# Kernel tuning notes

Measured on AMD Instinct MI355X. Metric: run time of the kernel, lower is better.

## Reference

```python
import jax, jax.numpy as jnp
import numpy as np
from jax import lax

D_MODEL = 512; N_HEADS = 32; HEAD_DIM = 16
D_INNER = 1024; D_STATE = 64; HDIM = 64; NH = 16; D_CONV = 4
CONV_CH = D_INNER + 2 * D_STATE          # 1152
D_INPROJ = 2 * D_INNER + 2 * D_STATE + NH  # 2192
B, L = 4, 1024


def setup_inputs() -> dict:
    key = jax.random.key(0)
    ks = jax.random.split(key, 16)
    def rn(k, shape, scale=0.02):
        return jax.random.normal(k, shape, jnp.float32) * scale
    inp = {"h": jax.random.normal(ks[0], (B, L, D_MODEL), jnp.float32)}
    inp["attn_in_w"] = rn(ks[1], (3 * D_MODEL, D_MODEL))
    inp["attn_in_b"] = jnp.zeros((3 * D_MODEL,), jnp.float32)
    inp["attn_out_w"] = rn(ks[2], (D_MODEL, D_MODEL))
    inp["attn_out_b"] = jnp.zeros((D_MODEL,), jnp.float32)
    i = 3
    for p in ("fwd", "bwd"):
        inp[f"{p}_inproj_w"] = rn(ks[i], (D_INPROJ, D_MODEL)); i += 1
        inp[f"{p}_conv_w"] = rn(ks[i], (CONV_CH, D_CONV), 0.1); i += 1
        inp[f"{p}_conv_b"] = jnp.zeros((CONV_CH,), jnp.float32)
        inp[f"{p}_dt_bias"] = rn(ks[i], (NH,), 0.5); i += 1
        inp[f"{p}_A_log"] = jnp.log(jax.random.uniform(ks[i], (NH,), jnp.float32, 1.0, 16.0)); i += 1
        inp[f"{p}_D"] = jnp.ones((NH,), jnp.float32)
        inp[f"{p}_norm_w"] = jnp.ones((D_INNER,), jnp.float32)
        inp[f"{p}_outproj_w"] = rn(ks[i], (D_MODEL, D_INNER)); i += 1
    inp["ln_w"] = jnp.ones((D_MODEL,), jnp.float32)
    inp["ln_b"] = jnp.zeros((D_MODEL,), jnp.float32)
    return inp


def _mha(h, in_w, in_b, out_w, out_b):
    b, l, d = h.shape
    qkv = h @ in_w.T + in_b
    q, k, v = jnp.split(qkv, 3, axis=-1)
    def heads(t):
        return t.reshape(b, l, N_HEADS, HEAD_DIM).transpose(0, 2, 1, 3)
    q, k, v = heads(q), heads(k), heads(v)
    scores = jnp.einsum('bhqd,bhkd->bhqk', q, k) * (1.0 / np.sqrt(HEAD_DIM))
    attn = jax.nn.softmax(scores, axis=-1)
    o = jnp.einsum('bhqk,bhkd->bhqd', attn, v).transpose(0, 2, 1, 3).reshape(b, l, d)
    return o @ out_w.T + out_b


def _causal_dwconv(x, w, bias):
    # x: (b, l, c), w: (c, k) depthwise causal conv
    xt = x.transpose(0, 2, 1)  # (b, c, l)
    out = lax.conv_general_dilated(xt, w[:, None, :], (1,), [(D_CONV - 1, 0)],
                                   feature_group_count=CONV_CH,
                                   dimension_numbers=('NCH', 'OIH', 'NCH'))
    return (out + bias[None, :, None]).transpose(0, 2, 1)


def _ssd(x, dt, A, Bm, Cm):
    # x: (b,l,nh,p), dt: (b,l,nh), Bm/Cm: (b,l,n) (ngroups=1)
    b = x.shape[0]
    dA = jnp.exp(dt * A)          # (b,l,nh)
    dtx = dt[..., None] * x       # (b,l,nh,p)
    def step(hst, inp):
        dA_t, dtx_t, B_t, C_t = inp
        hst = dA_t[:, :, None, None] * hst + dtx_t[..., None] * B_t[:, None, None, :]
        return hst, jnp.einsum('bhpn,bn->bhp', hst, C_t)
    init = jnp.zeros((b, NH, HDIM, D_STATE), x.dtype)
    _, ys = lax.scan(step, init, (dA.transpose(1, 0, 2), dtx.transpose(1, 0, 2, 3),
                                  Bm.transpose(1, 0, 2), Cm.transpose(1, 0, 2)))
    return ys.transpose(1, 0, 2, 3)  # (b,l,nh,p)


def _mamba2(u, inproj_w, conv_w, conv_b, dt_bias, A_log, Dp, norm_w, outproj_w):
    b, l, _ = u.shape
    zxbcdt = u @ inproj_w.T                      # (b,l,2192)
    z = zxbcdt[..., :D_INNER]
    xBC = zxbcdt[..., D_INNER:D_INNER + CONV_CH]
    dt = jax.nn.softplus(zxbcdt[..., D_INNER + CONV_CH:] + dt_bias)  # (b,l,nh)
    xBC = jax.nn.silu(_causal_dwconv(xBC, conv_w, conv_b))
    x = xBC[..., :D_INNER].reshape(b, l, NH, HDIM)
    Bm = xBC[..., D_INNER:D_INNER + D_STATE]
    Cm = xBC[..., D_INNER + D_STATE:]
    A = -jnp.exp(A_log)
    y = _ssd(x, dt, A, Bm, Cm) + Dp[None, None, :, None] * x
    y = y.reshape(b, l, D_INNER) * jax.nn.silu(z)  # gated (norm_before_gate=False)
    y = y * lax.rsqrt(jnp.mean(y * y, axis=-1, keepdims=True) + 1e-5) * norm_w  # RMSNormGated
    return y @ outproj_w.T


def reference(h, attn_in_w, attn_in_b, attn_out_w, attn_out_b,
              fwd_inproj_w, fwd_conv_w, fwd_conv_b, fwd_dt_bias, fwd_A_log, fwd_D, fwd_norm_w, fwd_outproj_w,
              bwd_inproj_w, bwd_conv_w, bwd_conv_b, bwd_dt_bias, bwd_A_log, bwd_D, bwd_norm_w, bwd_outproj_w,
              ln_w, ln_b):
    attn_out = _mha(h, attn_in_w, attn_in_b, attn_out_w, attn_out_b)
    fwd_out = _mamba2(h, fwd_inproj_w, fwd_conv_w, fwd_conv_b, fwd_dt_bias, fwd_A_log, fwd_D, fwd_norm_w, fwd_outproj_w)
    bwd_out = jnp.flip(_mamba2(jnp.flip(h, 1), bwd_inproj_w, bwd_conv_w, bwd_conv_b, bwd_dt_bias, bwd_A_log, bwd_D, bwd_norm_w, bwd_outproj_w), 1)
    s = h + attn_out + fwd_out + bwd_out
    mu = jnp.mean(s, axis=-1, keepdims=True)
    var = jnp.mean((s - mu) ** 2, axis=-1, keepdims=True)
    return (s - mu) * lax.rsqrt(var + 1e-5) * ln_w + ln_b
```

## Files before the change

kernel.cpp:

```cpp
#include <hip/hip_runtime.h>
#include <math.h>
#include <stdint.h>

#define B_ 4
#define L_ 1024
#define DM 512
#define NHA 32
#define HD 16
#define DI 1024
#define DSTATE 64
#define HDIM_ 64
#define NHM 16
#define DCONV 4
#define CONVCH 1152
#define DINPROJ 2192
#define NTOK (B_*L_)
#define QC 64
#define NC (L_/QC)
#define QKVS 5920

typedef __bf16 bf16x8 __attribute__((ext_vector_type(8)));
typedef float f32x4 __attribute__((ext_vector_type(4)));
typedef unsigned short ushort8 __attribute__((ext_vector_type(8)));
typedef unsigned short ushort4v __attribute__((ext_vector_type(4)));
typedef __fp16 fp16x2 __attribute__((ext_vector_type(2)));
typedef _Float16 f16x4 __attribute__((ext_vector_type(4)));
typedef _Float16 f16x8 __attribute__((ext_vector_type(8)));

__device__ __forceinline__ float siluf(float x) {
    return x / (1.0f + __expf(-x));
}

__device__ __forceinline__ unsigned short f2bf(float f) {
    unsigned u = __float_as_uint(f);
    unsigned r = (u + 0x7FFFu + ((u >> 16) & 1u)) >> 16;
    return (unsigned short)r;
}

__device__ __forceinline__ float bf2f(unsigned short u) {
    return __uint_as_float((unsigned)u << 16);
}

__device__ __forceinline__ void cvt8(const float* src, unsigned short* dst) {
    float4 a = ((const float4*)src)[0];
    float4 b = ((const float4*)src)[1];
    ushort8 o;
    o[0] = f2bf(a.x); o[1] = f2bf(a.y); o[2] = f2bf(a.z); o[3] = f2bf(a.w);
    o[4] = f2bf(b.x); o[5] = f2bf(b.y); o[6] = f2bf(b.z); o[7] = f2bf(b.w);
    *(ushort8*)dst = o;
}

__device__ __forceinline__ void gload16(const void* g, void* l) {
    auto gp = reinterpret_cast<const __attribute__((address_space(1))) unsigned int*>(
        reinterpret_cast<uintptr_t>(g));
    auto lp = reinterpret_cast<__attribute__((address_space(3))) unsigned int*>(
        reinterpret_cast<uintptr_t>(l));
    __builtin_amdgcn_global_load_lds(gp, lp, 16, 0, 0);
}

#define S0 262144
#define S1 (S0 + 98304)
#define S2 (S1 + 32768)
#define S3 (S2 + 140288)
#define S4 (S3 + 140288)
__global__ void cvt_all_kernel(const float* __restrict__ h, unsigned short* __restrict__ hB,
                               const float* __restrict__ w1, unsigned short* __restrict__ d1,
                               const float* __restrict__ w2, unsigned short* __restrict__ d2,
                               const float* __restrict__ w3, unsigned short* __restrict__ d3,
                               const float* __restrict__ w4, unsigned short* __restrict__ d4) {
    int i = blockIdx.x * blockDim.x + threadIdx.x;
    const float* src; unsigned short* dst; int off;
    if (i < S0)      { src = h;  dst = hB; off = i; }
    else if (i < S1) { src = w1; dst = d1; off = i - S0; }
    else if (i < S2) { src = w2; dst = d2; off = i - S1; }
    else if (i < S3) { src = w3; dst = d3; off = i - S2; }
    else             { src = w4; dst = d4; off = i - S3; }
    cvt8(src + (size_t)off * 8, dst + (size_t)off * 8);
}

__global__ void cvt_outproj_kernel(const float* __restrict__ fw, const float* __restrict__ bw,
                                   unsigned short* __restrict__ dst) {
    int i = blockIdx.x * blockDim.x + threadIdx.x;
    const int n8 = DM * DI / 8;
    int half = i >= n8;
    int off = half ? i - n8 : i;
    const float* src = half ? bw : fw;
    int e = off * 8;
    int r = e / DI, c = e % DI;
    cvt8(src + e, dst + (size_t)r * 2048 + half * 1024 + c);
}

template <int BN, bool OBF16, bool SWZ>
__global__ __launch_bounds__(256) void gemm_mfma_staged(
        const unsigned short* __restrict__ Ab, const unsigned short* __restrict__ Wb,
        const float* __restrict__ bias, int biasN, void* __restrict__ Cout,
        int M, int N, int K) {
    constexpr int BM = 128, BK = 32;
    constexpr int NF = BN / 32;
    constexpr int BLOADS = BN / 64;
    __shared__ unsigned short As[2][BM * BK];
    __shared__ unsigned short Bs[2][BN * BK];

    const int tid = threadIdx.x;
    const int wave = tid >> 6, lane = tid & 63;
    const int l15 = lane & 15, g = lane >> 4;
    const int wm = wave >> 1, wn = wave & 1;
    int m0, n0;
    if constexpr (SWZ) {
        int d = blockIdx.x;
        int xcd = d & 7, jj = d >> 3;
        n0 = (xcd * 6 + jj % 6) * BN;
        m0 = (jj / 6) * BM;
    } else {
        m0 = blockIdx.y * BM;
        n0 = blockIdx.x * BN;
    }

    f32x4 acc[4][NF];
    #pragma unroll
    for (int mi = 0; mi < 4; ++mi)
        #pragma unroll
        for (int nj = 0; nj < NF; ++nj) acc[mi][nj] = (f32x4){0.f, 0.f, 0.f, 0.f};

    auto stage = [&](int bufi, int k0) {
        #pragma unroll
        for (int i = 0; i < 2; ++i) {
            int c = (wave * 2 + i) * 64 + lane;
            int row = c >> 2;
            int kc = ((c & 3) ^ (row & 3)) * 8;
            gload16(Ab + (size_t)(m0 + row) * K + k0 + kc,
                    &As[bufi][(wave * 2 + i) * 64 * 8]);
        }
        #pragma unroll
        for (int i = 0; i < BLOADS; ++i) {
            int c = (wave * BLOADS + i) * 64 + lane;
            int row = c >> 2;
            int kc = ((c & 3) ^ (row & 3)) * 8;
            int rn = n0 + row; if (rn >= N) rn = N - 1;
            gload16(Wb + (size_t)rn * K + k0 + kc,
                    &Bs[bufi][(wave * BLOADS + i) * 64 * 8]);
        }
    };

    int cur = 0;
    stage(0, 0);
    __syncthreads();
    for (int k0 = 0; k0 < K; k0 += BK) {
        if (k0 + BK < K) stage(cur ^ 1, k0 + BK);
        const unsigned short* Ac = As[cur];
        const unsigned short* Bc = Bs[cur];
        bf16x8 af[4];
        #pragma unroll
        for (int mi = 0; mi < 4; ++mi) {
            int ar = wm * 64 + mi * 16 + l15;
            af[mi] = *(const bf16x8*)(Ac + ar * BK + ((g ^ (ar & 3)) * 8));
        }
        bf16x8 bfr[NF];
        #pragma unroll
        for (int nj = 0; nj < NF; ++nj) {
            int br = wn * (BN / 2) + nj * 16 + l15;
            bfr[nj] = *(const bf16x8*)(Bc + br * BK + ((g ^ (br & 3)) * 8));
        }
        #pragma unroll
        for (int mi = 0; mi < 4; ++mi)
            #pragma unroll
            for (int nj = 0; nj < NF; ++nj)
                acc[mi][nj] = __builtin_amdgcn_mfma_f32_16x16x32_bf16(af[mi], bfr[nj], acc[mi][nj], 0, 0, 0);
        __syncthreads();
        cur ^= 1;
    }

    #pragma unroll
    for (int mi = 0; mi < 4; ++mi) {
        int rbase = m0 + wm * 64 + mi * 16 + g * 4;
        #pragma unroll
        for (int nj = 0; nj < NF; ++nj) {
            int col = n0 + wn * (BN / 2) + nj * 16 + l15;
            if (col < N) {
                float bv = (bias && col < biasN) ? bias[col] : 0.f;
                #pragma unroll
                for (int r = 0; r < 4; ++r) {
                    float v = acc[mi][nj][r] + bv;
                    if constexpr (OBF16)
                        ((unsigned short*)Cout)[(size_t)(rbase + r) * N + col] = f2bf(v);
                    else
                        ((float*)Cout)[(size_t)(rbase + r) * N + col] = v;
                }
            }
        }
    }
}

#define KP 24
#define VP 132
__global__ __launch_bounds__(256) void attn_mfma_kernel(const unsigned short* __restrict__ qkv,
                                                        unsigned short* __restrict__ ob) {
    const int n = blockIdx.x;
    const int xcd = n & 7;
    const int j = n >> 3;
    const int bh = ((j >> 4) << 3) + xcd;
    const int qt = j & 15;
    const int h = bh & 31;
    const int b = bh >> 5;
    const int tid = threadIdx.x;
    const int wave = tid >> 6, lane = tid & 63;
    const int l15 = lane & 15, g = lane >> 4;

    __shared__ _Float16 Ksm[128 * KP];
    __shared__ _Float16 VsmT[16 * VP];

    const unsigned short* base = qkv + (size_t)b * L_ * QKVS;
    const int qrow = qt * 64 + wave * 16 + l15;

    f16x4 qf;
    {
        ushort4v qv = *(const ushort4v*)(base + (size_t)qrow * QKVS + h * 16 + g * 4);
        fp16x2 qa = __builtin_amdgcn_cvt_pkrtz(bf2f(qv[0]) * 0.25f, bf2f(qv[1]) * 0.25f);
        fp16x2 qb = __builtin_amdgcn_cvt_pkrtz(bf2f(qv[2]) * 0.25f, bf2f(qv[3]) * 0.25f);
        qf[0] = (_Float16)qa[0]; qf[1] = (_Float16)qa[1];
        qf[2] = (_Float16)qb[0]; qf[3] = (_Float16)qb[1];
    }
    f32x4 yacc = (f32x4){0.f, 0.f, 0.f, 0.f};
    float s = 0.f;

    const int sk = tid >> 1;
    const int sd = (tid & 1) * 8;

    for (int c0 = 0; c0 < L_; c0 += 128) {
        {
            ushort8 ka = *(const ushort8*)(base + (size_t)(c0 + sk) * QKVS + 512 + h * 16 + sd);
            fp16x2 k0 = __builtin_amdgcn_cvt_pkrtz(bf2f(ka[0]), bf2f(ka[1]));
            fp16x2 k1 = __builtin_amdgcn_cvt_pkrtz(bf2f(ka[2]), bf2f(ka[3]));
            fp16x2 k2 = __builtin_amdgcn_cvt_pkrtz(bf2f(ka[4]), bf2f(ka[5]));
            fp16x2 k3 = __builtin_amdgcn_cvt_pkrtz(bf2f(ka[6]), bf2f(ka[7]));
            f16x8 kv;
            kv[0] = (_Float16)k0[0]; kv[1] = (_Float16)k0[1];
            kv[2] = (_Float16)k1[0]; kv[3] = (_Float16)k1[1];
            kv[4] = (_Float16)k2[0]; kv[5] = (_Float16)k2[1];
            kv[6] = (_Float16)k3[0]; kv[7] = (_Float16)k3[1];
            *(f16x8*)(&Ksm[sk * KP + sd]) = kv;
            ushort8 va = *(const ushort8*)(base + (size_t)(c0 + sk) * QKVS + 1024 + h * 16 + sd);
            #pragma unroll
            for (int jj = 0; jj < 8; ++jj)
                VsmT[(sd + jj) * VP + sk] = (_Float16)bf2f(va[jj]);
        }
        __syncthreads();
        #pragma unroll
        for (int half = 0; half < 2; ++half) {
            f32x4 st[4];
            #pragma unroll
            for (int ks = 0; ks < 4; ++ks) {
                f16x4 kf = *(const f16x4*)(&Ksm[((half * 4 + ks) * 16 + l15) * KP + g * 4]);
                st[ks] = __builtin_amdgcn_mfma_f32_16x16x16f16(kf, qf, (f32x4){0.f,0.f,0.f,0.f}, 0, 0, 0);
            }
            float p[16];
            float cs = 0.f;
            #pragma unroll
            for (int ks = 0; ks < 4; ++ks) {
                #pragma unroll
                for (int r = 0; r < 4; ++r) {
                    p[ks * 4 + r] = __expf(st[ks][r]);
                    cs += p[ks * 4 + r];
                }
            }
            cs += __shfl_xor(cs, 16);
            cs += __shfl_xor(cs, 32);
            s += cs;
            #pragma unroll
            for (int ks = 0; ks < 4; ++ks) {
                fp16x2 plo = __builtin_amdgcn_cvt_pkrtz(p[ks*4+0], p[ks*4+1]);
                fp16x2 phi = __builtin_amdgcn_cvt_pkrtz(p[ks*4+2], p[ks*4+3]);
                f16x4 pf;
                pf[0] = (_Float16)plo[0]; pf[1] = (_Float16)plo[1];
                pf[2] = (_Float16)phi[0]; pf[3] = (_Float16)phi[1];
                f16x4 vf = *(const f16x4*)(&VsmT[l15 * VP + (half * 4 + ks) * 16 + g * 4]);
                yacc = __builtin_amdgcn_mfma_f32_16x16x16f16(vf, pf, yacc, 0, 0, 0);
            }
        }
        __syncthreads();
    }
    float inv = 1.f / s;
    ushort4v o;
    o[0] = f2bf(yacc[0] * inv);
    o[1] = f2bf(yacc[1] * inv);
    o[2] = f2bf(yacc[2] * inv);
    o[3] = f2bf(yacc[3] * inv);
    *(ushort4v*)(ob + (size_t)(b * L_ + qrow) * 512 + h * 16 + g * 4) = o;
}

__global__ void conv_silu_kernel(const unsigned short* __restrict__ megaA,
                                 const float* __restrict__ cw0, const float* __restrict__ cb0,
                                 const float* __restrict__ cw1, const float* __restrict__ cb1,
                                 unsigned short* __restrict__ out) {
    const int rev = blockIdx.y;
    const float* conv_w = rev ? cw1 : cw0;
    const float* conv_b = rev ? cb1 : cb0;
    int idx = blockIdx.x * blockDim.x + threadIdx.x;
    if (idx >= NTOK * (CONVCH / 4)) return;
    int c4 = (idx % (CONVCH / 4)) * 4;
    int bl = idx / (CONVCH / 4);
    int l = bl % L_;
    int b = bl / L_;
    const unsigned short* src = megaA + (size_t)b * L_ * QKVS + 1536 + rev * DINPROJ + 1024 + c4;
    float4 w0 = *(const float4*)(conv_w + (c4 + 0) * 4);
    float4 w1 = *(const float4*)(conv_w + (c4 + 1) * 4);
    float4 w2 = *(const float4*)(conv_w + (c4 + 2) * 4);
    float4 w3 = *(const float4*)(conv_w + (c4 + 3) * 4);
    float4 acc = *(const float4*)(conv_b + c4);
    const float wt[4][4] = {{w0.x, w0.y, w0.z, w0.w}, {w1.x, w1.y, w1.z, w1.w},
                            {w2.x, w2.y, w2.z, w2.w}, {w3.x, w3.y, w3.z, w3.w}};
    #pragma unroll
    for (int j = 0; j < 4; ++j) {
        int ll = rev ? (l + 3 - j) : (l - 3 + j);
        if (ll >= 0 && ll < L_) {
            ushort4v x = *(const ushort4v*)(src + (size_t)ll * QKVS);
            acc.x = fmaf(wt[0][j], bf2f(x[0]), acc.x);
            acc.y = fmaf(wt[1][j], bf2f(x[1]), acc.y);
            acc.z = fmaf(wt[2][j], bf2f(x[2]), acc.z);
            acc.w = fmaf(wt[3][j], bf2f(x[3]), acc.w);
        }
    }
    ushort4v o;
    o[0] = f2bf(siluf(acc.x)); o[1] = f2bf(siluf(acc.y));
    o[2] = f2bf(siluf(acc.z)); o[3] = f2bf(siluf(acc.w));
    *(ushort4v*)(out + (size_t)rev * NTOK * CONVCH + (size_t)bl * CONVCH + c4) = o;
}

__global__ void dt_exact_kernel(const float* __restrict__ h,
                                const float* __restrict__ wdt0, const float* __restrict__ bias0,
                                const float* __restrict__ wdt1, const float* __restrict__ bias1,
                                float* __restrict__ dt) {
    const int dir = blockIdx.y;
    const float* wdt = dir ? wdt1 : wdt0;
    const float* dbias = dir ? bias1 : bias0;
    const int row = blockIdx.x;
    const int tid = threadIdx.x;
    const int g = tid >> 4, j = tid & 15;
    const float* hr = h + (size_t)row * DM;
    const float* wr = wdt + (size_t)g * DM;
    float s = 0.f;
    #pragma unroll 8
    for (int t = 0; t < 32; ++t) {
        int k = j + t * 16;
        s = fmaf(hr[k], wr[k], s);
    }
    s += __shfl_xor(s, 1); s += __shfl_xor(s, 2);
    s += __shfl_xor(s, 4); s += __shfl_xor(s, 8);
    if (j == 0) {
        float v = s + dbias[g];
        dt[(size_t)dir * NTOK * NHM + (size_t)row * NHM + g] = (v > 20.f) ? v : log1pf(__expf(v));
    }
}

__global__ __launch_bounds__(256) void ssd_chunk_kernel(
        const unsigned short* __restrict__ xbcAll, const float* __restrict__ dtAll,
        const float* __restrict__ Al0, const float* __restrict__ Dp0,
        const float* __restrict__ Al1, const float* __restrict__ Dp1,
        unsigned short* __restrict__ y16, float* __restrict__ Sb0, float* __restrict__ Sb1,
        float* __restrict__ Edec) {
    const int dir = blockIdx.y;
    const int rev = dir;
    const unsigned short* xbc = xbcAll + (size_t)dir * NTOK * CONVCH;
    const float* dtb = dtAll + (size_t)dir * NTOK * NHM;
    float* Sbuf = dir ? Sb1 : Sb0;
    unsigned short* y = y16 + (size_t)dir * NTOK * DI;

    const int bid = blockIdx.x;
    const int q = bid & (NC - 1);
    const int bh = bid / NC;
    const int b = bh >> 4, h = bh & 15;
    const int tid = threadIdx.x;
    const int wave = tid >> 6, lane = tid & 63;
    const int l15 = lane & 15, l4 = lane >> 4;

    __shared__ unsigned short Bn[64 * 72];
    __shared__ unsigned short Cn[64 * 72];
    __shared__ unsigned short Btw[64 * 72];
    __shared__ unsigned short Gt[64 * 72];
    __shared__ unsigned short xT[64 * 72];
    __shared__ float sdt[QC], sc[QC], wsv[QC];

    const float A = -__expf((dir ? Al1 : Al0)[h]);
    const float Dh = (dir ? Dp1 : Dp0)[h];
    const int r = tid >> 2, qq = tid & 3;

    #pragma unroll
    for (int j = 0; j < 4; ++j) {
        int qd = qq + j * 4;
        int t = q * QC + r;
        int l = rev ? (L_ - 1 - t) : t;
        const unsigned short* rowp = xbc + (size_t)(b * L_ + l) * CONVCH;
        *(ushort4v*)&Bn[r * 72 + qd * 4] = *(const ushort4v*)(rowp + 1024 + qd * 4);
        *(ushort4v*)&Cn[r * 72 + qd * 4] = *(const ushort4v*)(rowp + 1088 + qd * 4);
    }
    if (tid < QC) {
        int t = q * QC + tid;
        int l = rev ? (L_ - 1 - t) : t;
        sdt[tid] = dtb[(size_t)(b * L_ + l) * NHM + h];
    }
    __syncthreads();
    if (tid == 0) {
        float run = 0.f;
        for (int i = 0; i < QC; ++i) { run += A * sdt[i]; sc[i] = run; }
    }
    __syncthreads();
    if (tid < QC) wsv[tid] = sdt[tid] * __expf(sc[QC - 1] - sc[tid]);
    if (tid == 0) Edec[dir * 1024 + bid] = __expf(sc[QC - 1]);
    __syncthreads();

    {
        int n = tid >> 2, s0 = (tid & 3) * 16;
        ushort8 o0, o1;
        #pragma unroll
        for (int k = 0; k < 8; ++k) {
            o0[k] = f2bf(bf2f(Bn[(s0 + k) * 72 + n]) * wsv[s0 + k]);
            o1[k] = f2bf(bf2f(Bn[(s0 + 8 + k) * 72 + n]) * wsv[s0 + 8 + k]);
        }
        *(ushort8*)&Btw[n * 72 + s0] = o0;
        *(ushort8*)&Btw[n * 72 + s0 + 8] = o1;
    }
    #pragma unroll
    for (int j = 0; j < 4; ++j) {
        int qd = qq + j * 4;
        int t = q * QC + r;
        int l = rev ? (L_ - 1 - t) : t;
        const unsigned short* rowp = xbc + (size_t)(b * L_ + l) * CONVCH + h * 64;
        ushort4v xv = *(const ushort4v*)(rowp + qd * 4);
        xT[(qd * 4 + 0) * 72 + r] = xv[0];
        xT[(qd * 4 + 1) * 72 + r] = xv[1];
        xT[(qd * 4 + 2) * 72 + r] = xv[2];
        xT[(qd * 4 + 3) * 72 + r] = xv[3];
    }
    __syncthreads();

    f32x4 accG[4];
    #pragma unroll
    for (int j = 0; j < 4; ++j) accG[j] = (f32x4){0.f, 0.f, 0.f, 0.f};
    #pragma unroll
    for (int k0 = 0; k0 < 64; k0 += 32) {
        bf16x8 af = *(const bf16x8*)&Bn[(wave * 16 + l15) * 72 + l4 * 8 + k0];
        #pragma unroll
        for (int j = 0; j < 4; ++j) {
            bf16x8 bfj = *(const bf16x8*)&Cn[(j * 16 + l15) * 72 + l4 * 8 + k0];
            accG[j] = __builtin_amdgcn_mfma_f32_16x16x32_bf16(af, bfj, accG[j], 0, 0, 0);
        }
    }
    #pragma unroll
    for (int j = 0; j < 4; ++j) {
        #pragma unroll
        for (int rr = 0; rr < 4; ++rr) {
            int s = wave * 16 + l4 * 4 + rr;
            int i = j * 16 + l15;
            float g = (s <= i) ? accG[j][rr] * sdt[s] * __expf(sc[i] - sc[s]) : 0.f;
            Gt[i * 72 + s] = f2bf(g);
        }
    }
    __syncthreads();

    {
        f32x4 accY[4];
        #pragma unroll
        for (int j = 0; j < 4; ++j) accY[j] = (f32x4){0.f, 0.f, 0.f, 0.f};
        #pragma unroll
        for (int k0 = 0; k0 < 64; k0 += 32) {
            bf16x8 af = *(const bf16x8*)&Gt[(wave * 16 + l15) * 72 + l4 * 8 + k0];
            #pragma unroll
            for (int j = 0; j < 4; ++j) {
                bf16x8 bfj = *(const bf16x8*)&xT[(j * 16 + l15) * 72 + l4 * 8 + k0];
                accY[j] = __builtin_amdgcn_mfma_f32_16x16x32_bf16(af, bfj, accY[j], 0, 0, 0);
            }
        }
        #pragma unroll
        for (int j = 0; j < 4; ++j) {
            #pragma unroll
            for (int rr = 0; rr < 4; ++rr) {
                int i = wave * 16 + l4 * 4 + rr;
                int p = j * 16 + l15;
                int t = q * QC + i;
                int l = rev ? (L_ - 1 - t) : t;
                float xv = bf2f(xT[p * 72 + i]);
                y[(size_t)(b * L_ + l) * DI + h * 64 + p] = f2bf(accY[j][rr] + Dh * xv);
            }
        }
    }
    {
        f32x4 accS[4];
        #pragma unroll
        for (int j = 0; j < 4; ++j) accS[j] = (f32x4){0.f, 0.f, 0.f, 0.f};
        #pragma unroll
        for (int k0 = 0; k0 < 64; k0 += 32) {
            bf16x8 af = *(const bf16x8*)&xT[(wave * 16 + l15) * 72 + l4 * 8 + k0];
            #pragma unroll
            for (int j = 0; j < 4; ++j) {
                bf16x8 bfj = *(const bf16x8*)&Btw[(j * 16 + l15) * 72 + l4 * 8 + k0];
                accS[j] = __builtin_amdgcn_mfma_f32_16x16x32_bf16(af, bfj, accS[j], 0, 0, 0);
            }
        }
        float* Sq = Sbuf + (size_t)bid * 4096;
        #pragma unroll
        for (int j = 0; j < 4; ++j) {
            #pragma unroll
            for (int rr = 0; rr < 4; ++rr) {
                int p = wave * 16 + l4 * 4 + rr;
                int n = j * 16 + l15;
                Sq[p * 64 + n] = accS[j][rr];
            }
        }
    }
}

__global__ void ssd_chain_kernel(float* __restrict__ Sb0, float* __restrict__ Sb1,
                                 const float* __restrict__ Edec) {
    const int dir = blockIdx.z;
    float* Sbuf = dir ? Sb1 : Sb0;
    const int bh = blockIdx.x;
    const int e = blockIdx.y * 256 + threadIdx.x;
    float* base = Sbuf + (size_t)bh * NC * 4096 + e;
    const float* Ep = Edec + dir * 1024 + bh * NC;
    float hst = 0.f;
    float tmp = base[0];
    #pragma unroll
    for (int q = 0; q < NC; ++q) {
        float nxt = (q + 1 < NC) ? base[(size_t)(q + 1) * 4096] : 0.f;
        float E = Ep[q];
        base[(size_t)q * 4096] = hst;
        hst = fmaf(E, hst, tmp);
        tmp = nxt;
    }
}

__global__ __launch_bounds__(256) void ssd_corr_kernel(
        const unsigned short* __restrict__ xbcAll, const float* __restrict__ dtAll,
        const float* __restrict__ Al0, const float* __restrict__ Al1,
        const float* __restrict__ Sb0, const float* __restrict__ Sb1,
        unsigned short* __restrict__ y16) {
    const int dir = blockIdx.y;
    const int rev = dir;
    const unsigned short* xbc = xbcAll + (size_t)dir * NTOK * CONVCH;
    const float* dtb = dtAll + (size_t)dir * NTOK * NHM;
    const float* Sbuf = dir ? Sb1 : Sb0;
    unsigned short* y = y16 + (size_t)dir * NTOK * DI;

    const int bid = blockIdx.x;
    const int q = bid & (NC - 1);
    const int bh = bid / NC;
    const int b = bh >> 4, h = bh & 15;
    const int tid = threadIdx.x;
    const int wave = tid >> 6, lane = tid & 63;
    const int l15 = lane & 15, l4 = lane >> 4;

    __shared__ unsigned short Cb[64 * 72];
    __shared__ unsigned short Hb[64 * 72];
    __shared__ float sdt[QC], sc[QC];
    const float A = -__expf((dir ? Al1 : Al0)[h]);
    const int r = tid >> 2, qq = tid & 3;
    const float* Sq = Sbuf + (size_t)bid * 4096;

    #pragma unroll
    for (int j = 0; j < 4; ++j) {
        int qd = qq + j * 4;
        int t = q * QC + r;
        int l = rev ? (L_ - 1 - t) : t;
        const unsigned short* rowp = xbc + (size_t)(b * L_ + l) * CONVCH;
        *(ushort4v*)&Cb[r * 72 + qd * 4] = *(const ushort4v*)(rowp + 1088 + qd * 4);
        float4 hv = ((const float4*)Sq)[r * 16 + qd];
        ushort4v hh;
        hh[0] = f2bf(hv.x); hh[1] = f2bf(hv.y); hh[2] = f2bf(hv.z); hh[3] = f2bf(hv.w);
        *(ushort4v*)&Hb[r * 72 + qd * 4] = hh;
    }
    if (tid < QC) {
        int t = q * QC + tid;
        int l = rev ? (L_ - 1 - t) : t;
        sdt[tid] = dtb[(size_t)(b * L_ + l) * NHM + h];
    }
    __syncthreads();
    if (tid == 0) {
        float run = 0.f;
        for (int i = 0; i < QC; ++i) { run += A * sdt[i]; sc[i] = run; }
    }
    __syncthreads();

    f32x4 acc[4];
    #pragma unroll
    for (int j = 0; j < 4; ++j) acc[j] = (f32x4){0.f, 0.f, 0.f, 0.f};
    #pragma unroll
    for (int k0 = 0; k0 < 64; k0 += 32) {
        bf16x8 af = *(const bf16x8*)&Cb[(wave * 16 + l15) * 72 + l4 * 8 + k0];
        #pragma unroll
        for (int j = 0; j < 4; ++j) {
            bf16x8 bfj = *(const bf16x8*)&Hb[(j * 16 + l15) * 72 + l4 * 8 + k0];
            acc[j] = __builtin_amdgcn_mfma_f32_16x16x32_bf16(af, bfj, acc[j], 0, 0, 0);
        }
    }
    #pragma unroll
    for (int j = 0; j < 4; ++j) {
        #pragma unroll
        for (int rr = 0; rr < 4; ++rr) {
            int i = wave * 16 + l4 * 4 + rr;
            int p = j * 16 + l15;
            int t = q * QC + i;
            int l = rev ? (L_ - 1 - t) : t;
            float e = __expf(sc[i]);
            unsigned short* yp = &y[(size_t)(b * L_ + l) * DI + h * 64 + p];
            *yp = f2bf(bf2f(*yp) + e * acc[j][rr]);
        }
    }
}

__global__ void gate_rmsnorm_kernel(const unsigned short* __restrict__ y16,
                                    const unsigned short* __restrict__ megaA,
                                    const float* __restrict__ nw0, const float* __restrict__ nw1,
                                    unsigned short* __restrict__ yb) {
    const int dir = blockIdx.y;
    const float* norm_w = dir ? nw1 : nw0;
    const int row = blockIdx.x;
    const int tid = threadIdx.x;
    const unsigned short* z = megaA + (size_t)row * QKVS + 1536 + dir * DINPROJ;
    const unsigned short* yr = y16 + (size_t)dir * NTOK * DI + (size_t)row * DI;
    float v[4];
    float ss = 0.f;
    #pragma unroll
    for (int i = 0; i < 4; ++i) {
        int c = i * 256 + tid;
        float g = siluf(bf2f(z[c]));
        v[i] = bf2f(yr[c]) * g;
        ss = fmaf(v[i], v[i], ss);
    }
    #pragma unroll
    for (int off = 32; off > 0; off >>= 1) ss += __shfl_xor(ss, off);
    __shared__ float red[4];
    int wid = tid >> 6, lane = tid & 63;
    if (lane == 0) red[wid] = ss;
    __syncthreads();
    ss = red[0] + red[1] + red[2] + red[3];
    float scale = rsqrtf(ss * (1.0f / 1024.0f) + 1e-5f);
    #pragma unroll
    for (int i = 0; i < 4; ++i) {
        int c = i * 256 + tid;
        yb[(size_t)row * 2048 + dir * 1024 + c] = f2bf(v[i] * scale * norm_w[c]);
    }
}

__global__ void final_ln_kernel(const float* __restrict__ h, const float* __restrict__ attn,
                                const float* __restrict__ msum,
                                const float* __restrict__ ln_w, const float* __restrict__ ln_b,
                                float* __restrict__ out) {
    const int row = blockIdx.x;
    const int tid = threadIdx.x;
    size_t base = (size_t)row * DM;
    float v[2];
    float sum = 0.f, sq = 0.f;
    #pragma unroll
    for (int i = 0; i < 2; ++i) {
        int c = i * 256 + tid;
        float s = h[base + c] + attn[base + c] + msum[base + c];
        v[i] = s;
        sum += s;
        sq = fmaf(s, s, sq);
    }
    #pragma unroll
    for (int off = 32; off > 0; off >>= 1) {
        sum += __shfl_xor(sum, off);
        sq += __shfl_xor(sq, off);
    }
    __shared__ float rsum[4], rsq[4];
    int wid = tid >> 6, lane = tid & 63;
    if (lane == 0) { rsum[wid] = sum; rsq[wid] = sq; }
    __syncthreads();
    sum = rsum[0] + rsum[1] + rsum[2] + rsum[3];
    sq = rsq[0] + rsq[1] + rsq[2] + rsq[3];
    float mu = sum * (1.0f / DM);
    float var = sq * (1.0f / DM) - mu * mu;
    float rs = rsqrtf(var + 1e-5f);
    #pragma unroll
    for (int i = 0; i < 2; ++i) {
        int c = i * 256 + tid;
        out[base + c] = (v[i] - mu) * rs * ln_w[c] + ln_b[c];
    }
}

extern "C" void kernel_launch(void* const* d_in, const int* in_sizes, int n_in,
                              void* d_out, int out_size, void* d_ws, size_t ws_size,
                              hipStream_t stream) {
    const float* h          = (const float*)d_in[0];
    const float* attn_in_w  = (const float*)d_in[1];
    const float* attn_in_b  = (const float*)d_in[2];
    const float* attn_out_w = (const float*)d_in[3];
    const float* attn_out_b = (const float*)d_in[4];
    const float* ln_w       = (const float*)d_in[21];
    const float* ln_b       = (const float*)d_in[22];
    float* out = (float*)d_out;

    float* ws = (float*)d_ws;
    unsigned short* megaA = (unsigned short*)ws;
    unsigned short* bufXBC = (unsigned short*)(ws + 12124160);
    float* bufDT   = ws + 12124160 + 4718592;
    float* bufY    = bufDT + 131072;
    float* bufATTN = bufY + 4194304;
    float* gateReg = bufATTN + 2097152;
    float* sReg    = gateReg + 4194304;
    float* bufEdec = sReg + 4194304;
    unsigned short* hB = (unsigned short*)(bufEdec + 2048);
    unsigned short* wBIG   = (unsigned short*)gateReg;
    unsigned short* wAOUT  = wBIG + (size_t)QKVS * DM;
    unsigned short* gatedB = (unsigned short*)gateReg;
    unsigned short* actB   = (unsigned short*)sReg;
    float* bufS0           = sReg;
    float* bufS1           = gateReg;
    unsigned short* wC     = (unsigned short*)sReg;
    unsigned short* y16    = (unsigned short*)bufY;
    float* msum            = bufY;

    const float* inproj_fwd = (const float*)d_in[5];
    const float* inproj_bwd = (const float*)d_in[13];

    dim3 blk(256);

    cvt_all_kernel<<<dim3(S4 / 256), blk, 0, stream>>>(
        h, hB, attn_in_w, wBIG, attn_out_w, wAOUT,
        inproj_fwd, wBIG + (size_t)1536 * DM, inproj_bwd, wBIG + (size_t)3728 * DM);

    gemm_mfma_staged<128, true, true><<<dim3(8 * 6 * (NTOK / 128)), blk, 0, stream>>>(
        hB, wBIG, attn_in_b, 1536, megaA, NTOK, QKVS, DM);

    attn_mfma_kernel<<<dim3(B_ * NHA * (L_ / 64)), blk, 0, stream>>>(megaA, actB);
    gemm_mfma_staged<64, false, false><<<dim3(DM / 64, NTOK / 128), blk, 0, stream>>>(
        actB, wAOUT, attn_out_b, DM, bufATTN, NTOK, DM, DM);

    dt_exact_kernel<<<dim3(NTOK, 2), blk, 0, stream>>>(
        h, inproj_fwd + (size_t)(DINPROJ - NHM) * DM, (const float*)d_in[8],
        inproj_bwd + (size_t)(DINPROJ - NHM) * DM, (const float*)d_in[16], bufDT);
    conv_silu_kernel<<<dim3((NTOK * (CONVCH / 4) + 255) / 256, 2), blk, 0, stream>>>(
        megaA, (const float*)d_in[6], (const float*)d_in[7],
        (const float*)d_in[14], (const float*)d_in[15], bufXBC);

    ssd_chunk_kernel<<<dim3(B_ * NHM * NC, 2), blk, 0, stream>>>(
        bufXBC, bufDT, (const float*)d_in[9], (const float*)d_in[10],
        (const float*)d_in[17], (const float*)d_in[18], y16, bufS0, bufS1, bufEdec);
    ssd_chain_kernel<<<dim3(B_ * NHM, 16, 2), blk, 0, stream>>>(bufS0, bufS1, bufEdec);
    ssd_corr_kernel<<<dim3(B_ * NHM * NC, 2), blk, 0, stream>>>(
        bufXBC, bufDT, (const float*)d_in[9], (const float*)d_in[17], bufS0, bufS1, y16);
    gate_rmsnorm_kernel<<<dim3(NTOK, 2), blk, 0, stream>>>(
        y16, megaA, (const float*)d_in[11], (const float*)d_in[19], gatedB);

    cvt_outproj_kernel<<<dim3((2 * DM * DI / 8 + 255) / 256), blk, 0, stream>>>(
        (const float*)d_in[12], (const float*)d_in[20], wC);
    gemm_mfma_staged<64, false, false><<<dim3(DM / 64, NTOK / 128), blk, 0, stream>>>(
        gatedB, wC, nullptr, 0, msum, NTOK, DM, 2048);

    final_ln_kernel<<<dim3(NTOK), blk, 0, stream>>>(
        h, bufATTN, msum, ln_w, ln_b, out);
}
```

Baseline: 238.9 us.

## Replace mega input-projection GEMM with 256x256 eight-phase pipelined MFMA kernel

Adds a new 512-thread GEMM kernel with 256x256 output tiles, 128KB of dynamic LDS double buffering, and an interleaved eight-phase schedule. The schedule alternates global-to-LDS staging, LDS fragment loads and MFMA groups, with sched barriers and setprio. It replaces the 128-tile staged GEMM for the fused QKV plus both in-projections. The aim is to overlap memory traffic with matrix math and raise per-block data reuse. The cost is a much smaller grid (384 blocks) and heavy register and LDS use, which may limit occupancy.

```diff
diff --git a/kernel.cpp b/kernel.cpp
--- a/kernel.cpp
+++ b/kernel.cpp
@@ -186,6 +186,168 @@
                     else
                         ((float*)Cout)[(size_t)(rbase + r) * N + col] = v;
                 }
+            }
+        }
+    }
+}
+
+#define PBAR() do { __builtin_amdgcn_sched_barrier(0); __builtin_amdgcn_s_barrier(); } while (0)
+#define MMAQ(MI0, BP, NJ0)                                                                   \
+    do {                                                                                     \
+        __builtin_amdgcn_s_setprio(1);                                                       \
+        _Pragma("unroll")                                                                    \
+        for (int i_ = 0; i_ < 4; ++i_) {                                                     \
+            _Pragma("unroll")                                                                \
+            for (int j_ = 0; j_ < 2; ++j_) {                                                 \
+                acc[(MI0)+i_][(NJ0)+j_] = __builtin_amdgcn_mfma_f32_16x16x32_bf16(           \
+                    af[i_][0], BP[j_][0], acc[(MI0)+i_][(NJ0)+j_], 0, 0, 0);                 \
+                acc[(MI0)+i_][(NJ0)+j_] = __builtin_amdgcn_mfma_f32_16x16x32_bf16(           \
+                    af[i_][1], BP[j_][1], acc[(MI0)+i_][(NJ0)+j_], 0, 0, 0);                 \
+            }                                                                                \
+        }                                                                                    \
+        __builtin_amdgcn_s_setprio(0);                                                       \
+    } while (0)
+
+__global__ __launch_bounds__(512, 2) void gemm_mega_8phase(
+        const unsigned short* __restrict__ Ab, const unsigned short* __restrict__ Wb,
+        const float* __restrict__ bias, int biasN, unsigned short* __restrict__ Cout,
+        int M, int Nreal, int K) {
+    extern __shared__ unsigned short lds[];
+    unsigned short* const LA = lds;
+    unsigned short* const LB = lds + 4 * 8192;
+
+    const int tid = threadIdx.x;
+    const int wave = tid >> 6, lane = tid & 63;
+    const int l15 = lane & 15, g4 = lane >> 4;
+    const int wm = wave >> 2, wn = wave & 3;
+
+    const int wg = blockIdx.x;
+    const int lin = (wg & 7) * 48 + (wg >> 3);
+    const int m0 = (lin & 15) * 256;
+    const int n0 = (lin >> 4) * 256;
+
+    f32x4 acc[8][4];
+    #pragma unroll
+    for (int i = 0; i < 8; ++i)
+        #pragma unroll
+        for (int j = 0; j < 4; ++j) acc[i][j] = (f32x4){0.f, 0.f, 0.f, 0.f};
+
+    auto stA = [&](int buf, int half, int kt) {
+        #pragma unroll
+        for (int i2 = 0; i2 < 2; ++i2) {
+            int c = (wave * 2 + i2) * 64 + lane;
+            int row = c >> 3, ch = c & 7;
+            gload16(Ab + (size_t)(m0 + half * 128 + row) * K + kt * 64 + ((ch ^ (row & 7)) * 8),
+                    LA + (buf * 2 + half) * 8192 + (wave * 2 + i2) * 512);
+        }
+    };
+    auto stB = [&](int buf, int half, int kt) {
+        #pragma unroll
+        for (int i2 = 0; i2 < 2; ++i2) {
+            int c = (wave * 2 + i2) * 64 + lane;
+            int row = c >> 3, ch = c & 7;
+            int rn = n0 + half * 128 + row;
+            if (rn >= Nreal) rn = Nreal - 1;
+            gload16(Wb + (size_t)rn * K + kt * 64 + ((ch ^ (row & 7)) * 8),
+                    LB + (buf * 2 + half) * 8192 + (wave * 2 + i2) * 512);
+        }
+    };
+
+    bf16x8 af[4][2], b01[2][2], b23[2][2];
+
+    auto ldA = [&](int buf, int miBase) {
+        #pragma unroll
+        for (int i = 0; i < 4; ++i) {
+            int r = (miBase + i) * 16 + l15;
+            #pragma unroll
+            for (int ks = 0; ks < 2; ++ks) {
+                int ch = ks * 4 + g4;
+                af[i][ks] = *(const bf16x8*)(LA + (buf * 2 + wm) * 8192 + r * 64 +
+                                             ((ch ^ (r & 7)) * 8));
+            }
+        }
+    };
+    auto ldB = [&](int buf, int njBase, bf16x8 (&bp)[2][2]) {
+        #pragma unroll
+        for (int j = 0; j < 2; ++j) {
+            int r = (wn & 1) * 64 + (njBase + j) * 16 + l15;
+            #pragma unroll
+            for (int ks = 0; ks < 2; ++ks) {
+                int ch = ks * 4 + g4;
+                bp[j][ks] = *(const bf16x8*)(LB + (buf * 2 + (wn >> 1)) * 8192 + r * 64 +
+                                             ((ch ^ (r & 7)) * 8));
+            }
+        }
+    };
+
+    stA(0, 0, 0); stA(0, 1, 0); stB(0, 0, 0); stB(0, 1, 0);
+    stB(1, 0, 1); stB(1, 1, 1);
+    asm volatile("s_waitcnt vmcnt(4)" ::: "memory");
+    PBAR();
+
+    const int NIT = K >> 7;
+    for (int it = 0; it < NIT; ++it) {
+        const int T1 = 2 * it + 1;
+        const bool st = (it + 1 < NIT);
+        ldA(0, 0); ldB(0, 0, b01);
+        stA(1, 0, T1);
+        PBAR();
+        MMAQ(0, b01, 0);
+        PBAR();
+        ldB(0, 2, b23);
+        stA(1, 1, T1);
+        PBAR();
+        MMAQ(0, b23, 2);
+        PBAR();
+        ldA(0, 4);
+        if (st) stB(0, 0, T1 + 1);
+        PBAR();
+        MMAQ(4, b23, 2);
+        PBAR();
+        if (st) {
+            stB(0, 1, T1 + 1);
+            asm volatile("s_waitcnt vmcnt(4)" ::: "memory");
+        } else {
+            asm volatile("s_waitcnt vmcnt(0)" ::: "memory");
+        }
+        PBAR();
+        MMAQ(4, b01, 0);
+        PBAR();
+        ldA(1, 0); ldB(1, 0, b01);
+        if (st) stA(0, 0, T1 + 1);
+        PBAR();
+        MMAQ(0, b01, 0);
+        PBAR();
+        ldB(1, 2, b23);
+        if (st) stA(0, 1, T1 + 1);
+        PBAR();
+        MMAQ(0, b23, 2);
+        PBAR();
+        ldA(1, 4);
+        if (st) stB(1, 0, T1 + 2);
+        PBAR();
+        MMAQ(4, b23, 2);
+        PBAR();
+        if (st) {
+            stB(1, 1, T1 + 2);
+            asm volatile("s_waitcnt vmcnt(4)" ::: "memory");
+        }
+        PBAR();
+        MMAQ(4, b01, 0);
+        PBAR();
+    }
+
+    #pragma unroll
+    for (int mi = 0; mi < 8; ++mi) {
+        int rbase = m0 + wm * 128 + mi * 16 + g4 * 4;
+        #pragma unroll
+        for (int nj = 0; nj < 4; ++nj) {
+            int col = n0 + wn * 64 + nj * 16 + l15;
+            if (col < Nreal) {
+                float bv = (col < biasN) ? bias[col] : 0.f;
+                #pragma unroll
+                for (int r = 0; r < 4; ++r)
+                    Cout[(size_t)(rbase + r) * Nreal + col] = f2bf(acc[mi][nj][r] + bv);
             }
         }
     }
@@ -720,7 +882,13 @@
         h, hB, attn_in_w, wBIG, attn_out_w, wAOUT,
         inproj_fwd, wBIG + (size_t)1536 * DM, inproj_bwd, wBIG + (size_t)3728 * DM);
 
-    gemm_mfma_staged<128, true, true><<<dim3(8 * 6 * (NTOK / 128)), blk, 0, stream>>>(
+    static bool smemSet = false;
+    if (!smemSet) {
+        (void)hipFuncSetAttribute(reinterpret_cast<const void*>(gemm_mega_8phase),
+                                  hipFuncAttributeMaxDynamicSharedMemorySize, 131072);
+        smemSet = true;
+    }
+    gemm_mega_8phase<<<dim3(16 * 24), dim3(512), 131072, stream>>>(
         hB, wBIG, attn_in_b, 1536, megaA, NTOK, QKVS, DM);
 
     attn_mfma_kernel<<<dim3(B_ * NHA * (L_ / 64)), blk, 0, stream>>>(megaA, actB);
```

Result: slower. 245.6 us (+2.8%).

## Replace mega QKV/inproj GEMM with triple-buffered 512-thread pipelined MFMA kernel

Applied to the files above, without the earlier changes.

Adds a new GEMM kernel for the large fused attention-QKV plus Mamba in-projection matmul. It uses 512 threads, 128x256 tiles, a three-stage LDS ring (144 KB dynamic shared memory) with async global-to-LDS loads issued two k-steps ahead, and split MFMA phases raised with s_setprio. Work-groups are remapped across XCDs for locality. The aim is to hide global load latency and raise MFMA utilisation. The cost is much higher LDS use, which limits occupancy, plus manual vmcnt bookkeeping that must match the number of loads in flight.

```diff
diff --git a/kernel.cpp b/kernel.cpp
--- a/kernel.cpp
+++ b/kernel.cpp
@@ -186,6 +186,135 @@
                     else
                         ((float*)Cout)[(size_t)(rbase + r) * N + col] = v;
                 }
+            }
+        }
+    }
+}
+
+#define MMAH(MI0)                                                                            \
+    do {                                                                                     \
+        __builtin_amdgcn_s_setprio(1);                                                       \
+        _Pragma("unroll")                                                                    \
+        for (int i_ = 0; i_ < 2; ++i_) {                                                     \
+            _Pragma("unroll")                                                                \
+            for (int j_ = 0; j_ < 4; ++j_) {                                                 \
+                acc[(MI0)+i_][j_] = __builtin_amdgcn_mfma_f32_16x16x32_bf16(                 \
+                    af[i_][0], bfr[j_][0], acc[(MI0)+i_][j_], 0, 0, 0);                      \
+                acc[(MI0)+i_][j_] = __builtin_amdgcn_mfma_f32_16x16x32_bf16(                 \
+                    af[i_][1], bfr[j_][1], acc[(MI0)+i_][j_], 0, 0, 0);                      \
+            }                                                                                \
+        }                                                                                    \
+        __builtin_amdgcn_s_setprio(0);                                                       \
+    } while (0)
+
+__global__ __launch_bounds__(512, 2) void gemm_mega_pipe(
+        const unsigned short* __restrict__ Ab, const unsigned short* __restrict__ Wb,
+        const float* __restrict__ bias, int biasN, unsigned short* __restrict__ Cout,
+        int M, int Nreal, int K) {
+    extern __shared__ unsigned short lds[];
+    unsigned short* const LA = lds;
+    unsigned short* const LB = lds + 3 * 8192;
+
+    const int tid = threadIdx.x;
+    const int wave = tid >> 6, lane = tid & 63;
+    const int l15 = lane & 15, g4 = lane >> 4;
+    const int wm = wave >> 2, wn = wave & 3;
+
+    const int wg = blockIdx.x;
+    const int lin = (wg & 7) * 96 + (wg >> 3);
+    const int m0 = (lin & 31) * 128;
+    const int n0 = (lin >> 5) * 256;
+
+    f32x4 acc[4][4];
+    #pragma unroll
+    for (int i = 0; i < 4; ++i)
+        #pragma unroll
+        for (int j = 0; j < 4; ++j) acc[i][j] = (f32x4){0.f, 0.f, 0.f, 0.f};
+
+    auto stA = [&](int buf, int kt) {
+        #pragma unroll
+        for (int i2 = 0; i2 < 2; ++i2) {
+            int c = (wave * 2 + i2) * 64 + lane;
+            int row = c >> 3, ch = c & 7;
+            gload16(Ab + (size_t)(m0 + row) * K + kt * 64 + ((ch ^ (row & 7)) * 8),
+                    LA + buf * 8192 + c * 8);
+        }
+    };
+    auto stB = [&](int buf, int half, int kt) {
+        #pragma unroll
+        for (int i2 = 0; i2 < 2; ++i2) {
+            int c = (wave * 2 + i2) * 64 + lane;
+            int row = c >> 3, ch = c & 7;
+            int rn = n0 + half * 128 + row;
+            if (rn >= Nreal) rn = Nreal - 1;
+            gload16(Wb + (size_t)rn * K + kt * 64 + ((ch ^ (row & 7)) * 8),
+                    LB + buf * 16384 + half * 8192 + c * 8);
+        }
+    };
+
+    bf16x8 af[2][2], bfr[4][2];
+    auto ldA2 = [&](int buf, int miBase) {
+        #pragma unroll
+        for (int i = 0; i < 2; ++i) {
+            int r = wm * 64 + (miBase + i) * 16 + l15;
+            #pragma unroll
+            for (int ks = 0; ks < 2; ++ks) {
+                int ch = ks * 4 + g4;
+                af[i][ks] = *(const bf16x8*)(LA + buf * 8192 + r * 64 + ((ch ^ (r & 7)) * 8));
+            }
+        }
+    };
+    auto ldB4 = [&](int buf) {
+        #pragma unroll
+        for (int j = 0; j < 4; ++j) {
+            int r = wn * 64 + j * 16 + l15;
+            #pragma unroll
+            for (int ks = 0; ks < 2; ++ks) {
+                int ch = ks * 4 + g4;
+                bfr[j][ks] = *(const bf16x8*)(LB + buf * 16384 + r * 64 + ((ch ^ (r & 7)) * 8));
+            }
+        }
+    };
+
+    stA(0, 0); stB(0, 0, 0); stB(0, 1, 0);
+    stA(1, 1); stB(1, 0, 1); stB(1, 1, 1);
+    asm volatile("s_waitcnt vmcnt(6)" ::: "memory");
+    __builtin_amdgcn_s_barrier();
+
+    const int NT = K >> 6;
+    int rb = 0;
+    for (int t = 0; t < NT; ++t) {
+        const bool st = (t + 2 < NT);
+        const int wb = (rb + 2 >= 3) ? rb - 1 : rb + 2;
+        ldA2(rb, 0); ldB4(rb);
+        if (st) { stA(wb, t + 2); stB(wb, 0, t + 2); }
+        __builtin_amdgcn_s_barrier();
+        MMAH(0);
+        __builtin_amdgcn_s_barrier();
+        ldA2(rb, 2);
+        if (st) {
+            stB(wb, 1, t + 2);
+            asm volatile("s_waitcnt vmcnt(6)" ::: "memory");
+        } else {
+            asm volatile("s_waitcnt vmcnt(0)" ::: "memory");
+        }
+        __builtin_amdgcn_s_barrier();
+        MMAH(2);
+        __builtin_amdgcn_s_barrier();
+        rb = (rb + 1 == 3) ? 0 : rb + 1;
+    }
+
+    #pragma unroll
+    for (int mi = 0; mi < 4; ++mi) {
+        int rbase = m0 + wm * 64 + mi * 16 + g4 * 4;
+        #pragma unroll
+        for (int nj = 0; nj < 4; ++nj) {
+            int col = n0 + wn * 64 + nj * 16 + l15;
+            if (col < Nreal) {
+                float bv = (col < biasN) ? bias[col] : 0.f;
+                #pragma unroll
+                for (int r = 0; r < 4; ++r)
+                    Cout[(size_t)(rbase + r) * Nreal + col] = f2bf(acc[mi][nj][r] + bv);
             }
         }
     }
@@ -720,7 +849,13 @@
         h, hB, attn_in_w, wBIG, attn_out_w, wAOUT,
         inproj_fwd, wBIG + (size_t)1536 * DM, inproj_bwd, wBIG + (size_t)3728 * DM);
 
-    gemm_mfma_staged<128, true, true><<<dim3(8 * 6 * (NTOK / 128)), blk, 0, stream>>>(
+    static bool smemSet = false;
+    if (!smemSet) {
+        (void)hipFuncSetAttribute(reinterpret_cast<const void*>(gemm_mega_pipe),
+                                  hipFuncAttributeMaxDynamicSharedMemorySize, 147456);
+        smemSet = true;
+    }
+    gemm_mega_pipe<<<dim3(768), dim3(512), 147456, stream>>>(
         hB, wBIG, attn_in_b, 1536, megaA, NTOK, QKVS, DM);
 
     attn_mfma_kernel<<<dim3(B_ * NHA * (L_ / 64)), blk, 0, stream>>>(megaA, actB);
```

Measured after the change: 244.1 us. 2.2% more time.
